# Kernel tuning notes

Hardware: AMD Instinct MI355X
Metric: run time of the kernel (lower is better)

The kernel has to match this reference:

```python
import jax, jax.numpy as jnp
import numpy as np

B, N, K, E, H, V = 128, 256, 4, 300, 150, 32000  # batch, nodes/tree, max children, embed, hidden, vocab
DELTA = 1.0


def setup_inputs() -> dict:
    key = jax.random.key(0)
    ks = jax.random.split(key, 8)
    query = jax.random.randint(ks[0], (B, N), 0, V, dtype=jnp.int32)
    pos = jax.random.randint(ks[1], (B, N), 0, V, dtype=jnp.int32)
    neg = jax.random.randint(ks[2], (B, N), 0, V, dtype=jnp.int32)
    # Complete K-ary tree over N nodes: children of node t are {K*t+1, ..., K*t+K} < N; root = node 0.
    ch = np.full((N, K), -1, dtype=np.int32)
    for t in range(N):
        for j in range(K):
            c = K * t + 1 + j
            if c < N:
                ch[t, j] = c
    children = jnp.asarray(ch)
    emb = jax.random.normal(ks[3], (V, E), dtype=jnp.float32) * 0.02
    W_iou = jax.random.normal(ks[4], (E, 3 * H), dtype=jnp.float32) * 0.05
    U_iou = jax.random.normal(ks[5], (H, 3 * H), dtype=jnp.float32) * 0.05
    b_iou = jnp.zeros((3 * H,), jnp.float32)
    W_f = jax.random.normal(ks[6], (E, H), dtype=jnp.float32) * 0.05
    U_f = jax.random.normal(ks[7], (H, H), dtype=jnp.float32) * 0.05
    b_f = jnp.zeros((H,), jnp.float32)
    return {"query": query, "pos": pos, "neg": neg, "children": children,
            "emb": emb, "W_iou": W_iou, "U_iou": U_iou, "b_iou": b_iou,
            "W_f": W_f, "U_f": U_f, "b_f": b_f}


def _childsum_treelstm(x, children, W_iou, U_iou, b_iou, W_f, U_f, b_f):
    """x: [B, N, E] node embeddings. Returns root (c, h): each [B, H]."""
    Bn, Nn, _ = x.shape
    Hh = U_f.shape[0]
    h0 = jnp.zeros((Bn, Nn, Hh), x.dtype)
    c0 = jnp.zeros((Bn, Nn, Hh), x.dtype)

    def step(carry, t):
        h_all, c_all = carry
        ch = children[t]                        # [K] child indices, -1 = padding
        mask = (ch >= 0)
        idx = jnp.where(mask, ch, 0)
        m = mask.astype(x.dtype)[None, :, None]  # [1, K, 1]
        h_k = h_all[:, idx] * m                 # [B, K, H]
        c_k = c_all[:, idx] * m
        h_sum = h_k.sum(axis=1)                 # child-sum h_tilde [B, H]
        x_t = x[:, t]                           # [B, E]
        iou = x_t @ W_iou + h_sum @ U_iou + b_iou
        i, o, u = jnp.split(iou, 3, axis=-1)
        i = jax.nn.sigmoid(i)
        o = jax.nn.sigmoid(o)
        u = jnp.tanh(u)
        # per-child forget gates: f_jk = sigmoid(W_f x_j + U_f h_k + b_f)
        f = jax.nn.sigmoid((x_t @ W_f + b_f)[:, None, :] + h_k @ U_f)  # [B, K, H]
        c_t = i * u + (f * c_k).sum(axis=1)     # c_k already masked
        h_t = o * jnp.tanh(c_t)
        return (h_all.at[:, t].set(h_t), c_all.at[:, t].set(c_t)), None

    # children have larger indices than parents -> process N-1 .. 0 (root last)
    (h_all, c_all), _ = jax.lax.scan(step, (h0, c0), jnp.arange(Nn - 1, -1, -1))
    return c_all[:, 0], h_all[:, 0]


def _cosine(a, b):
    num = (a * b).sum(-1)
    den = jnp.sqrt((a * a).sum(-1) * (b * b).sum(-1)) + 1e-8
    return num / den


def reference(query, pos, neg, children, emb, W_iou, U_iou, b_iou, W_f, U_f, b_f):
    qc, _ = _childsum_treelstm(emb[query], children, W_iou, U_iou, b_iou, W_f, U_f, b_f)
    pc, _ = _childsum_treelstm(emb[pos], children, W_iou, U_iou, b_iou, W_f, U_f, b_f)
    nc, _ = _childsum_treelstm(emb[neg], children, W_iou, U_iou, b_iou, W_f, U_f, b_f)
    a = _cosine(qc, pc)  # [B]
    b = _cosine(qc, nc)  # [B]
    return jax.nn.relu(DELTA - a + b)
```

## Files before the change

### kernel.cpp

```cpp
#include <hip/hip_runtime.h>
#include <hip/hip_bf16.h>

typedef short short8 __attribute__((ext_vector_type(8)));
typedef float floatx4 __attribute__((ext_vector_type(4)));
typedef unsigned short ushort;

#define Bb 128
#define Nn 256
#define Hh 150
#define HK 160
#define Vv 32000
#define NROW 384
#define PROJC 640
#define NINT 64
#define ZROW (Vv + NROW * NINT)

__device__ __forceinline__ float sigf(float x) { return 1.0f / (1.0f + __expf(-x)); }
__device__ __forceinline__ float tanhf_(float x) { return 1.0f - 2.0f / (__expf(2.0f * x) + 1.0f); }
__device__ __forceinline__ float bf2f(ushort s) { union { float f; unsigned u; } v; v.u = ((unsigned)s) << 16; return v.f; }
__device__ __forceinline__ ushort f2bf(float f) { __hip_bfloat16 h = __float2bfloat16(f); return *(ushort*)&h; }

__global__ __launch_bounds__(256) void k_prep(
    const float* __restrict__ W_iou, const float* __restrict__ W_f,
    const float* __restrict__ U_iou, const float* __restrict__ U_f,
    const float* __restrict__ b_iou, const float* __restrict__ b_f,
    short* __restrict__ Wt, short* __restrict__ Uti, short* __restrict__ Utf,
    float* __restrict__ biasw, ushort* __restrict__ h_u, float* __restrict__ c_u)
{
    int idx = blockIdx.x * 256 + threadIdx.x;
    const int nWt = 640 * 320, nUi = 464 * 160, nUf = 160 * 160;
    if (idx < nWt) {
        int n = idx / 320, k = idx % 320;
        int seg = n / 160, cc = n % 160;
        float v = 0.f;
        if (k < 300 && cc < 150) {
            if (seg == 0)      v = W_iou[k * 450 + cc];
            else if (seg == 1) v = W_iou[k * 450 + 150 + cc];
            else if (seg == 2) v = W_iou[k * 450 + 300 + cc];
            else               v = W_f[k * 150 + cc];
        }
        Wt[idx] = (short)f2bf(v);
    } else if (idx < nWt + nUi) {
        int i2 = idx - nWt; int n = i2 / 160, k = i2 % 160;
        float v = (k < 150 && n < 450) ? U_iou[k * 450 + n] : 0.f;
        Uti[i2] = (short)f2bf(v);
    } else if (idx < nWt + nUi + nUf) {
        int i2 = idx - nWt - nUi; int n = i2 / 160, k = i2 % 160;
        float v = (k < 150) ? U_f[k * 150 + n] : 0.f;
        Utf[i2] = (short)f2bf(v);
    } else if (idx < nWt + nUi + nUf + 640) {
        int n = idx - nWt - nUi - nUf;
        int seg = n / 160, cc = n % 160;
        biasw[n] = (cc < 150) ? (seg < 3 ? b_iou[seg * 150 + cc] : b_f[cc]) : 0.f;
    } else if (idx < nWt + nUi + nUf + 640 + HK) {
        int k = idx - (nWt + nUi + nUf + 640);
        h_u[(long)ZROW * HK + k] = 0;
        c_u[(long)ZROW * HK + k] = 0.f;
    }
}

__global__ __launch_bounds__(256) void k_vproj(
    const float* __restrict__ emb, const short* __restrict__ Wt,
    const float* __restrict__ biasw, ushort* __restrict__ proj,
    ushort* __restrict__ h_u, float* __restrict__ c_u)
{
    __shared__ __align__(16) short As[32 * 328];
    __shared__ __align__(16) float Tc[4][32][20];
    __shared__ __align__(16) ushort Th[4][32][24];
    ushort (*Tp)[32][72] = (ushort (*)[32][72])As;

    const int tid = threadIdx.x;
    const int v0 = blockIdx.x * 32;

    for (int i = tid; i < 32 * 80; i += 256) {
        int r = i / 80, q = i % 80, k0 = q * 4;
        short4 sv;
        if (k0 < 300) {
            float4 x = *(const float4*)(emb + (long)(v0 + r) * 300 + k0);
            sv.x = (short)f2bf(x.x); sv.y = (short)f2bf(x.y);
            sv.z = (short)f2bf(x.z); sv.w = (short)f2bf(x.w);
        } else sv = make_short4(0, 0, 0, 0);
        *(short4*)&As[r * 328 + k0] = sv;
    }
    __syncthreads();

    const int w = tid >> 6, lane = tid & 63;
    const int m = lane & 15, quad = lane >> 4, kq = quad * 8;

    short8 a0[10], a1[10];
    #pragma unroll
    for (int ks = 0; ks < 10; ks++) {
        a0[ks] = *(const short8*)&As[m * 328 + kq + ks * 32];
        a1[ks] = *(const short8*)&As[(16 + m) * 328 + kq + ks * 32];
    }
    __syncthreads();

    for (int j = w; j < 10; j += 4) {
        int col = j * 16 + m;
        const short* bp = Wt + (long)col * 320 + kq;
        floatx4 acc[4][2];
        #pragma unroll
        for (int s = 0; s < 4; s++) { acc[s][0] = {0.f,0.f,0.f,0.f}; acc[s][1] = {0.f,0.f,0.f,0.f}; }
        #pragma unroll
        for (int ks = 0; ks < 10; ks++) {
            short8 b0 = *(const short8*)(bp + 0 * 160 * 320 + ks * 32);
            short8 b1 = *(const short8*)(bp + 1 * 160 * 320 + ks * 32);
            short8 b2 = *(const short8*)(bp + 2 * 160 * 320 + ks * 32);
            short8 b3 = *(const short8*)(bp + 3 * 160 * 320 + ks * 32);
            acc[0][0] = __builtin_amdgcn_mfma_f32_16x16x32_bf16(a0[ks], b0, acc[0][0], 0, 0, 0);
            acc[0][1] = __builtin_amdgcn_mfma_f32_16x16x32_bf16(a1[ks], b0, acc[0][1], 0, 0, 0);
            acc[1][0] = __builtin_amdgcn_mfma_f32_16x16x32_bf16(a0[ks], b1, acc[1][0], 0, 0, 0);
            acc[1][1] = __builtin_amdgcn_mfma_f32_16x16x32_bf16(a1[ks], b1, acc[1][1], 0, 0, 0);
            acc[2][0] = __builtin_amdgcn_mfma_f32_16x16x32_bf16(a0[ks], b2, acc[2][0], 0, 0, 0);
            acc[2][1] = __builtin_amdgcn_mfma_f32_16x16x32_bf16(a1[ks], b2, acc[2][1], 0, 0, 0);
            acc[3][0] = __builtin_amdgcn_mfma_f32_16x16x32_bf16(a0[ks], b3, acc[3][0], 0, 0, 0);
            acc[3][1] = __builtin_amdgcn_mfma_f32_16x16x32_bf16(a1[ks], b3, acc[3][1], 0, 0, 0);
        }

        float bias[4] = { biasw[col], biasw[160 + col], biasw[320 + col], biasw[480 + col] };
        float pre[4][2][4];
        #pragma unroll
        for (int s = 0; s < 4; s++)
            #pragma unroll
            for (int g = 0; g < 2; g++)
                #pragma unroll
                for (int reg = 0; reg < 4; reg++)
                    pre[s][g][reg] = acc[s][g][reg] + bias[s];

        #pragma unroll
        for (int g = 0; g < 2; g++)
            #pragma unroll
            for (int reg = 0; reg < 4; reg++) {
                int rr = g * 16 + quad * 4 + reg;
                #pragma unroll
                for (int s = 0; s < 4; s++)
                    Tp[w][rr][s * 16 + m] = f2bf(pre[s][g][reg]);
                float iv = sigf(pre[0][g][reg]);
                float ov = sigf(pre[1][g][reg]);
                float uv = tanhf_(pre[2][g][reg]);
                float cc = iv * uv;
                Tc[w][rr][m] = cc;
                Th[w][rr][m] = f2bf(ov * tanhf_(cc));
            }
        asm volatile("s_waitcnt lgkmcnt(0)" ::: "memory");
        {
            int row = lane >> 1, half = lane & 1;
            long rowv = v0 + row;
            #pragma unroll
            for (int s2 = 0; s2 < 2; s2++) {
                int s = half * 2 + s2;
                int4 p0 = *(const int4*)&Tp[w][row][s * 16];
                int4 p1 = *(const int4*)&Tp[w][row][s * 16 + 8];
                *(int4*)(proj + rowv * PROJC + s * 160 + j * 16)     = p0;
                *(int4*)(proj + rowv * PROJC + s * 160 + j * 16 + 8) = p1;
            }
            int4 hv = *(const int4*)&Th[w][row][half * 8];
            *(int4*)(h_u + rowv * HK + j * 16 + half * 8) = hv;
            #pragma unroll
            for (int qq = half; qq < 4; qq += 2) {
                float4 cv4 = *(const float4*)&Tc[w][row][qq * 4];
                *(float4*)(c_u + rowv * HK + j * 16 + qq * 4) = cv4;
            }
        }
        asm volatile("s_waitcnt lgkmcnt(0)" ::: "memory");
    }
}

__global__ __launch_bounds__(256) void k_level(
    int t0, int G,
    const int* __restrict__ tq, const int* __restrict__ tp, const int* __restrict__ tn,
    const int* __restrict__ children, const ushort* __restrict__ proj,
    const short* __restrict__ Uti, const short* __restrict__ Utf,
    ushort* __restrict__ h_u, float* __restrict__ c_u)
{
    __shared__ __align__(16) short As[5][16][168];
    __shared__ __align__(16) float Cs[4][16][164];
    __shared__ int idx_s[16][4];
    __shared__ int tok_s[16];

    const int tid = threadIdx.x;
    const int gi = blockIdx.x % G;
    const int rest = blockIdx.x / G;
    const int t = t0 + rest / 24;
    const int r0 = (rest % 24) * 16;

    if (tid < 64) {
        int r = tid >> 2, j = tid & 3;
        int rg = r0 + r, g = rg >> 7, b = rg & 127;
        const int* tok = (g == 0) ? tq : (g == 1 ? tp : tn);
        int ch = children[t * 4 + j];
        int idx;
        if (ch < 0)        idx = ZROW;
        else if (ch >= 64) idx = tok[b * Nn + ch];
        else               idx = Vv + rg * NINT + ch;
        idx_s[r][j] = idx;
        if (j == 0) tok_s[r] = tok[b * Nn + t];
    }
    __syncthreads();

    for (int i = tid; i < 16 * 20; i += 256) {
        int r = i / 20, k0 = (i % 20) * 8;
        int4 v0 = *(const int4*)(h_u + (long)idx_s[r][0] * HK + k0);
        int4 v1 = *(const int4*)(h_u + (long)idx_s[r][1] * HK + k0);
        int4 v2 = *(const int4*)(h_u + (long)idx_s[r][2] * HK + k0);
        int4 v3 = *(const int4*)(h_u + (long)idx_s[r][3] * HK + k0);
        *(int4*)&As[1][r][k0] = v0;
        *(int4*)&As[2][r][k0] = v1;
        *(int4*)&As[3][r][k0] = v2;
        *(int4*)&As[4][r][k0] = v3;
        ushort s[8];
        const ushort* p0 = (const ushort*)&v0; const ushort* p1 = (const ushort*)&v1;
        const ushort* p2 = (const ushort*)&v2; const ushort* p3 = (const ushort*)&v3;
        #pragma unroll
        for (int e = 0; e < 8; e++)
            s[e] = f2bf(bf2f(p0[e]) + bf2f(p1[e]) + bf2f(p2[e]) + bf2f(p3[e]));
        *(int4*)&As[0][r][k0] = *(int4*)s;
    }
    for (int i = tid; i < 16 * 40; i += 256) {
        int r = i / 40, k0 = (i % 40) * 4;
        #pragma unroll
        for (int j = 0; j < 4; j++)
            *(float4*)&Cs[j][r][k0] = *(const float4*)(c_u + (long)idx_s[r][j] * HK + k0);
    }
    __syncthreads();

    const int w = tid >> 6, lane = tid & 63;
    const int m = lane & 15, kq = (lane >> 4) * 8;
    const int rbase = (lane >> 4) * 4;

    for (int nt = gi * 4 + w; nt < 10; nt += 4 * G) {
        int col = nt * 16 + m;
        const short* bi  = Uti + (long)(col) * HK + kq;
        const short* bo  = Uti + (long)(150 + col) * HK + kq;
        const short* bu  = Uti + (long)(300 + col) * HK + kq;
        const short* bff = Utf + (long)col * HK + kq;
        floatx4 ai = {0.f,0.f,0.f,0.f}, ao = ai, au = ai;
        floatx4 af0 = ai, af1 = ai, af2 = ai, af3 = ai;
        #pragma unroll
        for (int ks = 0; ks < 5; ks++) {
            short8 asum = *(const short8*)&As[0][m][kq + ks * 32];
            short8 ac0  = *(const short8*)&As[1][m][kq + ks * 32];
            short8 ac1  = *(const short8*)&As[2][m][kq + ks * 32];
            short8 ac2  = *(const short8*)&As[3][m][kq + ks * 32];
            short8 ac3  = *(const short8*)&As[4][m][kq + ks * 32];
            short8 vbi = *(const short8*)(bi + ks * 32);
            short8 vbo = *(const short8*)(bo + ks * 32);
            short8 vbu = *(const short8*)(bu + ks * 32);
            short8 vbf = *(const short8*)(bff + ks * 32);
            ai  = __builtin_amdgcn_mfma_f32_16x16x32_bf16(asum, vbi, ai, 0, 0, 0);
            ao  = __builtin_amdgcn_mfma_f32_16x16x32_bf16(asum, vbo, ao, 0, 0, 0);
            au  = __builtin_amdgcn_mfma_f32_16x16x32_bf16(asum, vbu, au, 0, 0, 0);
            af0 = __builtin_amdgcn_mfma_f32_16x16x32_bf16(ac0,  vbf, af0, 0, 0, 0);
            af1 = __builtin_amdgcn_mfma_f32_16x16x32_bf16(ac1,  vbf, af1, 0, 0, 0);
            af2 = __builtin_amdgcn_mfma_f32_16x16x32_bf16(ac2,  vbf, af2, 0, 0, 0);
            af3 = __builtin_amdgcn_mfma_f32_16x16x32_bf16(ac3,  vbf, af3, 0, 0, 0);
        }

        if (col < Hh) {
            #pragma unroll
            for (int reg = 0; reg < 4; reg++) {
                int r = rbase + reg, rg = r0 + r;
                const ushort* pr = proj + (long)tok_s[r] * PROJC;
                float iv = sigf(bf2f(pr[col])        + ai[reg]);
                float ov = sigf(bf2f(pr[160 + col])  + ao[reg]);
                float uv = tanhf_(bf2f(pr[320 + col]) + au[reg]);
                float fpre = bf2f(pr[480 + col]);
                float cv = iv * uv;
                cv = fmaf(sigf(fpre + af0[reg]), Cs[0][r][col], cv);
                cv = fmaf(sigf(fpre + af1[reg]), Cs[1][r][col], cv);
                cv = fmaf(sigf(fpre + af2[reg]), Cs[2][r][col], cv);
                cv = fmaf(sigf(fpre + af3[reg]), Cs[3][r][col], cv);
                long o = (long)(Vv + rg * NINT + t) * HK + col;
                c_u[o] = cv;
                h_u[o] = f2bf(ov * tanhf_(cv));
            }
        } else {
            #pragma unroll
            for (int reg = 0; reg < 4; reg++) {
                long o = (long)(Vv + (r0 + rbase + reg) * NINT + t) * HK + col;
                c_u[o] = 0.f; h_u[o] = 0;
            }
        }
    }
}

__global__ __launch_bounds__(64) void k_cos(const float* __restrict__ c_u, float* __restrict__ out)
{
    int b = blockIdx.x, tid = threadIdx.x;
    const float* qc = c_u + (long)(Vv + (0 * Bb + b) * NINT) * HK;
    const float* pc = c_u + (long)(Vv + (1 * Bb + b) * NINT) * HK;
    const float* nc = c_u + (long)(Vv + (2 * Bb + b) * NINT) * HK;
    float qp = 0, qn = 0, qq = 0, pp = 0, nn2 = 0;
    for (int k = tid; k < Hh; k += 64) {
        float qv = qc[k], pv = pc[k], nv = nc[k];
        qp += qv * pv; qn += qv * nv; qq += qv * qv; pp += pv * pv; nn2 += nv * nv;
    }
    #pragma unroll
    for (int off = 32; off > 0; off >>= 1) {
        qp += __shfl_down(qp, off, 64);
        qn += __shfl_down(qn, off, 64);
        qq += __shfl_down(qq, off, 64);
        pp += __shfl_down(pp, off, 64);
        nn2 += __shfl_down(nn2, off, 64);
    }
    if (tid == 0) {
        float a = qp / (sqrtf(qq * pp) + 1e-8f);
        float d = qn / (sqrtf(qq * nn2) + 1e-8f);
        out[b] = fmaxf(0.0f, 1.0f - a + d);
    }
}

extern "C" void kernel_launch(void* const* d_in, const int* in_sizes, int n_in,
                              void* d_out, int out_size, void* d_ws, size_t ws_size,
                              hipStream_t stream)
{
    const int*   tq       = (const int*)d_in[0];
    const int*   tp       = (const int*)d_in[1];
    const int*   tn       = (const int*)d_in[2];
    const int*   children = (const int*)d_in[3];
    const float* emb      = (const float*)d_in[4];
    const float* W_iou    = (const float*)d_in[5];
    const float* U_iou    = (const float*)d_in[6];
    const float* b_iou    = (const float*)d_in[7];
    const float* W_f      = (const float*)d_in[8];
    const float* U_f      = (const float*)d_in[9];
    const float* b_f      = (const float*)d_in[10];
    float* out = (float*)d_out;

    char* ws = (char*)d_ws;
    ushort* proj  = (ushort*)ws;
    ushort* h_u   = (ushort*)(ws + 40960000);
    float*  c_u   = (float*)(ws + 59064640);
    short*  Wt    = (short*)(ws + 95273920);
    short*  Uti   = (short*)(ws + 95683520);
    short*  Utf   = (short*)(ws + 95832000);
    float*  biasw = (float*)(ws + 95883200);

    k_prep<<<1194, 256, 0, stream>>>(W_iou, W_f, U_iou, U_f, b_iou, b_f,
                                     Wt, Uti, Utf, biasw, h_u, c_u);
    k_vproj<<<Vv / 32, 256, 0, stream>>>(emb, Wt, biasw, proj, h_u, c_u);
    k_level<<<43 * 24 * 1, 256, 0, stream>>>(21, 1, tq, tp, tn, children, proj, Uti, Utf, h_u, c_u);
    k_level<<<16 * 24 * 2, 256, 0, stream>>>(5,  2, tq, tp, tn, children, proj, Uti, Utf, h_u, c_u);
    k_level<<<4 * 24 * 3, 256, 0, stream>>>(1,   3, tq, tp, tn, children, proj, Uti, Utf, h_u, c_u);
    k_level<<<1 * 24 * 3, 256, 0, stream>>>(0,   3, tq, tp, tn, children, proj, Uti, Utf, h_u, c_u);
    k_cos<<<Bb, 64, 0, stream>>>(c_u, out);
}
```

Baseline: 274.2 us.

## Project only internal-node tokens into MFMA-fragment layout; leaf kernel skips full proj

Replaces the full-vocabulary 640-column projection table with two kernels. A leaf kernel computes only the i/o/u gates per vocab row and writes h/c. A separate kernel projects just the 64 internal-node tokens per tree instance into a buffer laid out in MFMA accumulator order. The level kernels then read their input pre-activations as contiguous uint2 loads instead of gathering scattered bf16 values by token id, and the vocab pass drops its large proj write. The cost is an extra launch and an extra gather of embedding rows for the internal nodes.

Result: slower. 284.9 us (+3.9%).

```diff
diff --git a/kernel.cpp b/kernel.cpp
--- a/kernel.cpp
+++ b/kernel.cpp
@@ -11,7 +11,6 @@
 #define HK 160
 #define Vv 32000
 #define NROW 384
-#define PROJC 640
 #define NINT 64
 #define ZROW (Vv + NROW * NINT)
 
@@ -59,16 +58,14 @@
     }
 }
 
-__global__ __launch_bounds__(256) void k_vproj(
+__global__ __launch_bounds__(256) void k_vleafproj(
     const float* __restrict__ emb, const short* __restrict__ Wt,
-    const float* __restrict__ biasw, ushort* __restrict__ proj,
+    const float* __restrict__ biasw,
     ushort* __restrict__ h_u, float* __restrict__ c_u)
 {
     __shared__ __align__(16) short As[32 * 328];
     __shared__ __align__(16) float Tc[4][32][20];
     __shared__ __align__(16) ushort Th[4][32][24];
-    ushort (*Tp)[32][72] = (ushort (*)[32][72])As;
-
     const int tid = threadIdx.x;
     const int v0 = blockIdx.x * 32;
 
@@ -93,7 +90,90 @@
         a0[ks] = *(const short8*)&As[m * 328 + kq + ks * 32];
         a1[ks] = *(const short8*)&As[(16 + m) * 328 + kq + ks * 32];
     }
+
+    for (int j = w; j < 10; j += 4) {
+        int col = j * 16 + m;
+        const short* bp = Wt + (long)col * 320 + kq;
+        floatx4 acc[3][2];
+        #pragma unroll
+        for (int s = 0; s < 3; s++) { acc[s][0] = {0.f,0.f,0.f,0.f}; acc[s][1] = {0.f,0.f,0.f,0.f}; }
+        #pragma unroll
+        for (int ks = 0; ks < 10; ks++) {
+            short8 b0 = *(const short8*)(bp + 0 * 160 * 320 + ks * 32);
+            short8 b1 = *(const short8*)(bp + 1 * 160 * 320 + ks * 32);
+            short8 b2 = *(const short8*)(bp + 2 * 160 * 320 + ks * 32);
+            acc[0][0] = __builtin_amdgcn_mfma_f32_16x16x32_bf16(a0[ks], b0, acc[0][0], 0, 0, 0);
+            acc[0][1] = __builtin_amdgcn_mfma_f32_16x16x32_bf16(a1[ks], b0, acc[0][1], 0, 0, 0);
+            acc[1][0] = __builtin_amdgcn_mfma_f32_16x16x32_bf16(a0[ks], b1, acc[1][0], 0, 0, 0);
+            acc[1][1] = __builtin_amdgcn_mfma_f32_16x16x32_bf16(a1[ks], b1, acc[1][1], 0, 0, 0);
+            acc[2][0] = __builtin_amdgcn_mfma_f32_16x16x32_bf16(a0[ks], b2, acc[2][0], 0, 0, 0);
+            acc[2][1] = __builtin_amdgcn_mfma_f32_16x16x32_bf16(a1[ks], b2, acc[2][1], 0, 0, 0);
+        }
+
+        float bi_ = biasw[col], bo_ = biasw[160 + col], bu_ = biasw[320 + col];
+        #pragma unroll
+        for (int g = 0; g < 2; g++)
+            #pragma unroll
+            for (int reg = 0; reg < 4; reg++) {
+                float iv = sigf(acc[0][g][reg] + bi_);
+                float ov = sigf(acc[1][g][reg] + bo_);
+                float uv = tanhf_(acc[2][g][reg] + bu_);
+                float cc = iv * uv;
+                int rr = g * 16 + quad * 4 + reg;
+                Tc[w][rr][m] = cc;
+                Th[w][rr][m] = f2bf(ov * tanhf_(cc));
+            }
+        asm volatile("s_waitcnt lgkmcnt(0)" ::: "memory");
+        {
+            int row = lane >> 1, half = lane & 1;
+            long rowv = v0 + row;
+            int4 hv = *(const int4*)&Th[w][row][half * 8];
+            *(int4*)(h_u + rowv * HK + j * 16 + half * 8) = hv;
+            #pragma unroll
+            for (int qq = half; qq < 4; qq += 2) {
+                float4 cv4 = *(const float4*)&Tc[w][row][qq * 4];
+                *(float4*)(c_u + rowv * HK + j * 16 + qq * 4) = cv4;
+            }
+        }
+        asm volatile("s_waitcnt lgkmcnt(0)" ::: "memory");
+    }
+}
+
+__global__ __launch_bounds__(256) void k_iproj(
+    const int* __restrict__ tq, const int* __restrict__ tp, const int* __restrict__ tn,
+    const float* __restrict__ emb, const short* __restrict__ Wt,
+    const float* __restrict__ biasw, ushort* __restrict__ ipre)
+{
+    __shared__ __align__(16) short As[32 * 328];
+    const int tid = threadIdx.x;
+    const int iblk = blockIdx.x;
+
+    for (int i = tid; i < 32 * 80; i += 256) {
+        int r = i / 80, q = i % 80, k0 = q * 4;
+        int inst = iblk * 32 + r;
+        int t = inst / 384, rg = inst % 384;
+        int g3 = rg >> 7, b = rg & 127;
+        const int* tok = (g3 == 0) ? tq : (g3 == 1 ? tp : tn);
+        int v = tok[b * Nn + t];
+        short4 sv;
+        if (k0 < 300) {
+            float4 x = *(const float4*)(emb + (long)v * 300 + k0);
+            sv.x = (short)f2bf(x.x); sv.y = (short)f2bf(x.y);
+            sv.z = (short)f2bf(x.z); sv.w = (short)f2bf(x.w);
+        } else sv = make_short4(0, 0, 0, 0);
+        *(short4*)&As[r * 328 + k0] = sv;
+    }
     __syncthreads();
+
+    const int w = tid >> 6, lane = tid & 63;
+    const int m = lane & 15, kq = (lane >> 4) * 8;
+
+    short8 a0[10], a1[10];
+    #pragma unroll
+    for (int ks = 0; ks < 10; ks++) {
+        a0[ks] = *(const short8*)&As[m * 328 + kq + ks * 32];
+        a1[ks] = *(const short8*)&As[(16 + m) * 328 + kq + ks * 32];
+    }
 
     for (int j = w; j < 10; j += 4) {
         int col = j * 16 + m;
@@ -118,65 +198,28 @@
         }
 
         float bias[4] = { biasw[col], biasw[160 + col], biasw[320 + col], biasw[480 + col] };
-        float pre[4][2][4];
+        long tbase = (long)(iblk * 10 + j) * 2048;
         #pragma unroll
         for (int s = 0; s < 4; s++)
             #pragma unroll
-            for (int g = 0; g < 2; g++)
-                #pragma unroll
-                for (int reg = 0; reg < 4; reg++)
-                    pre[s][g][reg] = acc[s][g][reg] + bias[s];
-
-        #pragma unroll
-        for (int g = 0; g < 2; g++)
-            #pragma unroll
-            for (int reg = 0; reg < 4; reg++) {
-                int rr = g * 16 + quad * 4 + reg;
-                #pragma unroll
-                for (int s = 0; s < 4; s++)
-                    Tp[w][rr][s * 16 + m] = f2bf(pre[s][g][reg]);
-                float iv = sigf(pre[0][g][reg]);
-                float ov = sigf(pre[1][g][reg]);
-                float uv = tanhf_(pre[2][g][reg]);
-                float cc = iv * uv;
-                Tc[w][rr][m] = cc;
-                Th[w][rr][m] = f2bf(ov * tanhf_(cc));
+            for (int g = 0; g < 2; g++) {
+                unsigned u0 = (unsigned)f2bf(acc[s][g][0] + bias[s]) | ((unsigned)f2bf(acc[s][g][1] + bias[s]) << 16);
+                unsigned u1 = (unsigned)f2bf(acc[s][g][2] + bias[s]) | ((unsigned)f2bf(acc[s][g][3] + bias[s]) << 16);
+                *(uint2*)(ipre + tbase + s * 512 + g * 256 + lane * 4) = make_uint2(u0, u1);
             }
-        asm volatile("s_waitcnt lgkmcnt(0)" ::: "memory");
-        {
-            int row = lane >> 1, half = lane & 1;
-            long rowv = v0 + row;
-            #pragma unroll
-            for (int s2 = 0; s2 < 2; s2++) {
-                int s = half * 2 + s2;
-                int4 p0 = *(const int4*)&Tp[w][row][s * 16];
-                int4 p1 = *(const int4*)&Tp[w][row][s * 16 + 8];
-                *(int4*)(proj + rowv * PROJC + s * 160 + j * 16)     = p0;
-                *(int4*)(proj + rowv * PROJC + s * 160 + j * 16 + 8) = p1;
-            }
-            int4 hv = *(const int4*)&Th[w][row][half * 8];
-            *(int4*)(h_u + rowv * HK + j * 16 + half * 8) = hv;
-            #pragma unroll
-            for (int qq = half; qq < 4; qq += 2) {
-                float4 cv4 = *(const float4*)&Tc[w][row][qq * 4];
-                *(float4*)(c_u + rowv * HK + j * 16 + qq * 4) = cv4;
-            }
-        }
-        asm volatile("s_waitcnt lgkmcnt(0)" ::: "memory");
     }
 }
 
 __global__ __launch_bounds__(256) void k_level(
     int t0, int G,
     const int* __restrict__ tq, const int* __restrict__ tp, const int* __restrict__ tn,
-    const int* __restrict__ children, const ushort* __restrict__ proj,
+    const int* __restrict__ children, const ushort* __restrict__ ipre,
     const short* __restrict__ Uti, const short* __restrict__ Utf,
     ushort* __restrict__ h_u, float* __restrict__ c_u)
 {
     __shared__ __align__(16) short As[5][16][168];
     __shared__ __align__(16) float Cs[4][16][164];
     __shared__ int idx_s[16][4];
-    __shared__ int tok_s[16];
 
     const int tid = threadIdx.x;
     const int gi = blockIdx.x % G;
@@ -194,7 +237,6 @@
         else if (ch >= 64) idx = tok[b * Nn + ch];
         else               idx = Vv + rg * NINT + ch;
         idx_s[r][j] = idx;
-        if (j == 0) tok_s[r] = tok[b * Nn + t];
     }
     __syncthreads();
 
@@ -227,6 +269,8 @@
     const int w = tid >> 6, lane = tid & 63;
     const int m = lane & 15, kq = (lane >> 4) * 8;
     const int rbase = (lane >> 4) * 4;
+    const long pblk = (long)((t * 384 + r0) >> 5) * 10;
+    const int pg_off = ((r0 >> 4) & 1) * 256 + lane * 4;
 
     for (int nt = gi * 4 + w; nt < 10; nt += 4 * G) {
         int col = nt * 16 + m;
@@ -257,14 +301,22 @@
         }
 
         if (col < Hh) {
+            const ushort* pb = ipre + (pblk + nt) * 2048 + pg_off;
+            uint2 pi = *(const uint2*)(pb + 0 * 512);
+            uint2 po = *(const uint2*)(pb + 1 * 512);
+            uint2 pu = *(const uint2*)(pb + 2 * 512);
+            uint2 pf = *(const uint2*)(pb + 3 * 512);
+            const ushort* pis = (const ushort*)&pi;
+            const ushort* pos = (const ushort*)&po;
+            const ushort* pus = (const ushort*)&pu;
+            const ushort* pfs = (const ushort*)&pf;
             #pragma unroll
             for (int reg = 0; reg < 4; reg++) {
                 int r = rbase + reg, rg = r0 + r;
-                const ushort* pr = proj + (long)tok_s[r] * PROJC;
-                float iv = sigf(bf2f(pr[col])        + ai[reg]);
-                float ov = sigf(bf2f(pr[160 + col])  + ao[reg]);
-                float uv = tanhf_(bf2f(pr[320 + col]) + au[reg]);
-                float fpre = bf2f(pr[480 + col]);
+                float iv = sigf(bf2f(pis[reg])   + ai[reg]);
+                float ov = sigf(bf2f(pos[reg])   + ao[reg]);
+                float uv = tanhf_(bf2f(pus[reg]) + au[reg]);
+                float fpre = bf2f(pfs[reg]);
                 float cv = iv * uv;
                 cv = fmaf(sigf(fpre + af0[reg]), Cs[0][r][col], cv);
                 cv = fmaf(sigf(fpre + af1[reg]), Cs[1][r][col], cv);
@@ -328,20 +380,21 @@
     float* out = (float*)d_out;
 
     char* ws = (char*)d_ws;
-    ushort* proj  = (ushort*)ws;
-    ushort* h_u   = (ushort*)(ws + 40960000);
-    float*  c_u   = (float*)(ws + 59064640);
-    short*  Wt    = (short*)(ws + 95273920);
-    short*  Uti   = (short*)(ws + 95683520);
-    short*  Utf   = (short*)(ws + 95832000);
-    float*  biasw = (float*)(ws + 95883200);
+    ushort* ipre  = (ushort*)ws;
+    ushort* h_u   = (ushort*)(ws + 31457280);
+    float*  c_u   = (float*)(ws + 49561920);
+    short*  Wt    = (short*)(ws + 85771200);
+    short*  Uti   = (short*)(ws + 86180800);
+    short*  Utf   = (short*)(ws + 86329280);
+    float*  biasw = (float*)(ws + 86380480);
 
     k_prep<<<1194, 256, 0, stream>>>(W_iou, W_f, U_iou, U_f, b_iou, b_f,
                                      Wt, Uti, Utf, biasw, h_u, c_u);
-    k_vproj<<<Vv / 32, 256, 0, stream>>>(emb, Wt, biasw, proj, h_u, c_u);
-    k_level<<<43 * 24 * 1, 256, 0, stream>>>(21, 1, tq, tp, tn, children, proj, Uti, Utf, h_u, c_u);
-    k_level<<<16 * 24 * 2, 256, 0, stream>>>(5,  2, tq, tp, tn, children, proj, Uti, Utf, h_u, c_u);
-    k_level<<<4 * 24 * 3, 256, 0, stream>>>(1,   3, tq, tp, tn, children, proj, Uti, Utf, h_u, c_u);
-    k_level<<<1 * 24 * 3, 256, 0, stream>>>(0,   3, tq, tp, tn, children, proj, Uti, Utf, h_u, c_u);
+    k_iproj<<<768, 256, 0, stream>>>(tq, tp, tn, emb, Wt, biasw, ipre);
+    k_vleafproj<<<Vv / 32, 256, 0, stream>>>(emb, Wt, biasw, h_u, c_u);
+    k_level<<<43 * 24 * 1, 256, 0, stream>>>(21, 1, tq, tp, tn, children, ipre, Uti, Utf, h_u, c_u);
+    k_level<<<16 * 24 * 2, 256, 0, stream>>>(5,  2, tq, tp, tn, children, ipre, Uti, Utf, h_u, c_u);
+    k_level<<<4 * 24 * 3, 256, 0, stream>>>(1,   3, tq, tp, tn, children, ipre, Uti, Utf, h_u, c_u);
+    k_level<<<1 * 24 * 3, 256, 0, stream>>>(0,   3, tq, tp, tn, children, ipre, Uti, Utf, h_u, c_u);
     k_cos<<<Bb, 64, 0, stream>>>(c_u, out);
 }
```
